# Kernel tuning notes

Measured on AMD Instinct MI355X. Metric: run time of the kernel, lower is better.

Reference implementation:

```python
import jax, jax.numpy as jnp
import numpy as np


def lga_once(x, w, r):
    """One pass of local guided aggregation (GANet LGA).

    x: [B, D, H, W] cost volume
    w: [B, 3*k*k, H, W] per-pixel guidance weights (k = 2r+1); the three
       k*k groups weight disparity planes d, d-1, d+1 respectively.
    out[b,d,h,w] = sum_{i,j in kxk window}
        w0[b,ij,h,w] * x[b, d,   h+i-r, w+j-r]
      + w1[b,ij,h,w] * x[b, d-1, h+i-r, w+j-r]
      + w2[b,ij,h,w] * x[b, d+1, h+i-r, w+j-r]
    with zero padding outside spatial and disparity bounds.
    """
    B, D, H, W = x.shape
    k = 2 * r + 1
    k2 = k * k
    w0 = w[:, 0 * k2:1 * k2]
    w1 = w[:, 1 * k2:2 * k2]
    w2 = w[:, 2 * k2:3 * k2]
    # disparity-shifted volumes: xm[:, d] = x[:, d-1], xp[:, d] = x[:, d+1]
    xm = jnp.pad(x, ((0, 0), (1, 0), (0, 0), (0, 0)))[:, :D]
    xp = jnp.pad(x, ((0, 0), (0, 1), (0, 0), (0, 0)))[:, 1:]
    spad = ((0, 0), (0, 0), (r, r), (r, r))
    x0p = jnp.pad(x, spad)
    xmp = jnp.pad(xm, spad)
    xpp = jnp.pad(xp, spad)
    out = jnp.zeros_like(x)
    idx = 0
    for i in range(k):          # small fixed kxk loop; data dims stay vectorized
        for j in range(k):
            p0 = x0p[:, :, i:i + H, j:j + W]
            pm = xmp[:, :, i:i + H, j:j + W]
            pp = xpp[:, :, i:i + H, j:j + W]
            out = out + (w0[:, idx:idx + 1] * p0
                         + w1[:, idx:idx + 1] * pm
                         + w2[:, idx:idx + 1] * pp)
            idx += 1
    return out


def setup_inputs() -> dict:
    key = jax.random.key(0)
    k1, k2 = jax.random.split(key)
    B, D, H, W = 2, 48, 320, 640
    r = 2
    kk = 2 * r + 1
    input1 = jax.random.normal(k1, (B, D, H, W), dtype=jnp.float32)
    input2 = jax.random.uniform(k2, (B, 3 * kk * kk, H, W), dtype=jnp.float32)
    return {"input1": input1, "input2": input2, "radius": r}


def reference(input1, input2, radius):
    # LGA2 = local guided aggregation applied twice with the same weights
    y = lga_once(input1, input2, radius)
    return lga_once(y, input2, radius)
```

## Files before the change

kernel.cpp:

```cpp
#include <hip/hip_runtime.h>

namespace {
constexpr int Bn = 2, Dn = 48, Hn = 320, Wn = 640;
constexpr int R = 2, K = 5, K2 = 25, C3 = 75;
constexpr int TW = 64, TH = 4;
constexpr int LW = TW + 2 * R;
constexpr int LH = TH + 2 * R;
constexpr int NT = TW * TH;
constexpr int LTOT = LH * LW;
constexpr int LTOTP = 576;
constexpr int NSLOT = 8;
}

#define BARRIER(N) \
    asm volatile("s_waitcnt vmcnt(" #N ") lgkmcnt(0)\n\ts_barrier" ::: "memory")

__global__ __launch_bounds__(NT, 2)
void lga_pass(const float* __restrict__ x, const float* __restrict__ wt,
              float* __restrict__ out) {
    __shared__ __align__(16) float pl[NSLOT][LTOTP];

    const int tx = threadIdx.x;
    const int ty = threadIdx.y;
    const int tid = ty * TW + tx;

    const int w0pix = blockIdx.x * TW;
    const int h0pix = blockIdx.y * TH;
    const int b = blockIdx.z;

    const int gw = w0pix + tx;
    const int gh = h0pix + ty;

    const size_t ps = (size_t)Hn * Wn;

    int soff[3];
#pragma unroll
    for (int t = 0; t < 3; ++t) {
        int idx = tid + t * NT;
        int rr = idx / LW;
        int cc = idx - rr * LW;
        int hh = h0pix - R + rr;
        int ww = w0pix - R + cc;
        bool ok = (idx < LTOT) && hh >= 0 && hh < Hn && ww >= 0 && ww < Wn;
        soff[t] = ok ? (hh * Wn + ww) : 0;
    }

    const float* xb = x + (size_t)b * Dn * ps;
    const int wseg = tid & ~63;

    float wr[C3];
    {
        const float* wp = wt + (size_t)b * C3 * ps + (size_t)gh * Wn + gw;
#pragma unroll
        for (int c = 0; c < C3; ++c) wr[c] = wp[(size_t)c * ps];
#pragma unroll
        for (int i = 0; i < K; ++i) {
            const int hh = gh + i - R;
            const bool vh = (hh >= 0) && (hh < Hn);
#pragma unroll
            for (int j = 0; j < K; ++j) {
                const int ww = gw + j - R;
                if (!(vh && ww >= 0 && ww < Wn)) {
                    wr[i * K + j] = 0.f;
                    wr[K2 + i * K + j] = 0.f;
                    wr[2 * K2 + i * K + j] = 0.f;
                }
            }
        }
    }

    float* op = out + (size_t)b * Dn * ps + (size_t)gh * Wn + gw;
    const int lbase = ty * LW + tx;

    auto dma = [&](int p, int slot) {
        if (p >= Dn) return;
        const float* src = xb + (size_t)p * ps;
        __builtin_amdgcn_global_load_lds(
            (const __attribute__((address_space(1))) void*)(src + soff[0]),
            (__attribute__((address_space(3))) void*)(&pl[slot][0 * NT + wseg]),
            4, 0, 0);
        __builtin_amdgcn_global_load_lds(
            (const __attribute__((address_space(1))) void*)(src + soff[1]),
            (__attribute__((address_space(3))) void*)(&pl[slot][1 * NT + wseg]),
            4, 0, 0);
        if (ty == 0) {
            __builtin_amdgcn_global_load_lds(
                (const __attribute__((address_space(1))) void*)(src + soff[2]),
                (__attribute__((address_space(3))) void*)(&pl[slot][2 * NT + tx]),
                4, 0, 0);
        }
    };

    float carry = 0.f, s1prev = 0.f;

    auto step = [&](int p, int sR, int sD) {
        dma(p + 6, sD);
        float S0 = 0.f, S1 = 0.f, S2 = 0.f;
#pragma unroll
        for (int i = 0; i < K; ++i) {
            float v0 = pl[sR][lbase + i * LW + 0];
            float v1 = pl[sR][lbase + i * LW + 1];
            float v2 = pl[sR][lbase + i * LW + 2];
            float v3 = pl[sR][lbase + i * LW + 3];
            float v4 = pl[sR][lbase + i * LW + 4];
            S0 += wr[i*K+0]*v0 + wr[i*K+1]*v1 + wr[i*K+2]*v2 + wr[i*K+3]*v3 + wr[i*K+4]*v4;
            S1 += wr[K2+i*K+0]*v0 + wr[K2+i*K+1]*v1 + wr[K2+i*K+2]*v2 + wr[K2+i*K+3]*v3 + wr[K2+i*K+4]*v4;
            S2 += wr[2*K2+i*K+0]*v0 + wr[2*K2+i*K+1]*v1 + wr[2*K2+i*K+2]*v2 + wr[2*K2+i*K+3]*v3 + wr[2*K2+i*K+4]*v4;
        }
        if (p > 0) { *op = carry + S2; op += ps; }
        carry = S0 + s1prev;
        s1prev = S1;
    };

#pragma unroll
    for (int q = 0; q < 6; ++q) dma(q, q);
    BARRIER(8);

    for (int d0 = 0; d0 < 40; d0 += 8) {
        step(d0 + 0, 0, 6); step(d0 + 1, 1, 7); BARRIER(8);
        step(d0 + 2, 2, 0); step(d0 + 3, 3, 1); BARRIER(8);
        step(d0 + 4, 4, 2); step(d0 + 5, 5, 3); BARRIER(8);
        step(d0 + 6, 6, 4); step(d0 + 7, 7, 5); BARRIER(8);
    }
    step(40, 0, 6); step(41, 1, 7); BARRIER(8);
    step(42, 2, 0); step(43, 3, 1); BARRIER(4);
    step(44, 4, 2); step(45, 5, 3); BARRIER(0);
    step(46, 6, 4); step(47, 7, 5);
    *op = carry;
}

extern "C" void kernel_launch(void* const* d_in, const int* in_sizes, int n_in,
                              void* d_out, int out_size, void* d_ws, size_t ws_size,
                              hipStream_t stream) {
    const float* x = (const float*)d_in[0];
    const float* w = (const float*)d_in[1];
    float* out = (float*)d_out;
    float* tmp = (float*)d_ws;

    dim3 block(TW, TH, 1);
    dim3 grid(Wn / TW, Hn / TH, Bn);

    lga_pass<<<grid, block, 0, stream>>>(x, w, tmp);
    lga_pass<<<grid, block, 0, stream>>>(tmp, w, out);
}
```

Measured before the change: 380.4 us.

## Interleave disparity plane pairs as float2 in LDS to halve reads per plane

The shared-memory tile now holds two consecutive disparity planes interleaved as float2 in each slot. Each global_load_lds lane pair fetches the same pixel from adjacent planes. Each compute step reads one float2 per tap and accumulates two planes at once, which halves LDS read instructions and barriers per plane. The pipeline is rebuilt with 6 double-plane slots, new vmcnt thresholds, and a changed output-ordering scheme where the first step's S2a is written to plane D-1. This relies on the wraparound indexing and waitcnt counts being exactly right.

```diff
diff --git a/kernel.cpp b/kernel.cpp
--- a/kernel.cpp
+++ b/kernel.cpp
@@ -5,11 +5,10 @@
 constexpr int R = 2, K = 5, K2 = 25, C3 = 75;
 constexpr int TW = 64, TH = 4;
 constexpr int LW = TW + 2 * R;
-constexpr int LH = TH + 2 * R;
 constexpr int NT = TW * TH;
-constexpr int LTOT = LH * LW;
-constexpr int LTOTP = 576;
-constexpr int NSLOT = 8;
+constexpr int LTOT = 544;
+constexpr int SPAD = 640;
+constexpr int NSLOT = 6;
 }
 
 #define BARRIER(N) \
@@ -18,11 +17,10 @@
 __global__ __launch_bounds__(NT, 2)
 void lga_pass(const float* __restrict__ x, const float* __restrict__ wt,
               float* __restrict__ out) {
-    __shared__ __align__(16) float pl[NSLOT][LTOTP];
+    __shared__ float2 pl2[NSLOT][SPAD];
 
     const int tx = threadIdx.x;
     const int ty = threadIdx.y;
-    const int tid = ty * TW + tx;
 
     const int w0pix = blockIdx.x * TW;
     const int h0pix = blockIdx.y * TH;
@@ -33,20 +31,20 @@
 
     const size_t ps = (size_t)Hn * Wn;
 
-    int soff[3];
+    int soffA[5];
 #pragma unroll
-    for (int t = 0; t < 3; ++t) {
-        int idx = tid + t * NT;
-        int rr = idx / LW;
-        int cc = idx - rr * LW;
+    for (int t = 0; t < 5; ++t) {
+        int s = ty * 160 + t * 32 + (tx >> 1);
+        int rr = s / LW;
+        int cc = s - rr * LW;
         int hh = h0pix - R + rr;
         int ww = w0pix - R + cc;
-        bool ok = (idx < LTOT) && hh >= 0 && hh < Hn && ww >= 0 && ww < Wn;
-        soff[t] = ok ? (hh * Wn + ww) : 0;
+        bool ok = (s < LTOT) && hh >= 0 && hh < Hn && ww >= 0 && ww < Wn;
+        soffA[t] = ok ? (hh * Wn + ww) : 0;
     }
 
     const float* xb = x + (size_t)b * Dn * ps;
-    const int wseg = tid & ~63;
+    const float* xq = xb + (size_t)(tx & 1) * ps;
 
     float wr[C3];
     {
@@ -72,60 +70,60 @@
     float* op = out + (size_t)b * Dn * ps + (size_t)gh * Wn + gw;
     const int lbase = ty * LW + tx;
 
-    auto dma = [&](int p, int slot) {
-        if (p >= Dn) return;
-        const float* src = xb + (size_t)p * ps;
-        __builtin_amdgcn_global_load_lds(
-            (const __attribute__((address_space(1))) void*)(src + soff[0]),
-            (__attribute__((address_space(3))) void*)(&pl[slot][0 * NT + wseg]),
-            4, 0, 0);
-        __builtin_amdgcn_global_load_lds(
-            (const __attribute__((address_space(1))) void*)(src + soff[1]),
-            (__attribute__((address_space(3))) void*)(&pl[slot][1 * NT + wseg]),
-            4, 0, 0);
-        if (ty == 0) {
+    auto dma = [&](const float* pbase, int slot) {
+#pragma unroll
+        for (int t = 0; t < 5; ++t) {
             __builtin_amdgcn_global_load_lds(
-                (const __attribute__((address_space(1))) void*)(src + soff[2]),
-                (__attribute__((address_space(3))) void*)(&pl[slot][2 * NT + tx]),
+                (const __attribute__((address_space(1))) void*)(pbase + soffA[t]),
+                (__attribute__((address_space(3))) void*)(&pl2[slot][ty * 160 + t * 32]),
                 4, 0, 0);
         }
     };
 
     float carry = 0.f, s1prev = 0.f;
+    const float* pref = xq;
 
-    auto step = [&](int p, int sR, int sD) {
-        dma(p + 6, sD);
-        float S0 = 0.f, S1 = 0.f, S2 = 0.f;
+    dma(pref, 0); pref += 2 * ps;
+    dma(pref, 1); pref += 2 * ps;
+    dma(pref, 2); pref += 2 * ps;
+
+    auto stepc = [&](int slot, bool issue, bool first) {
+        if (issue) { dma(pref, (slot + 3 >= NSLOT) ? slot - 3 : slot + 3); pref += 2 * ps; }
+        float S0a = 0.f, S1a = 0.f, S2a = 0.f;
+        float S0b = 0.f, S1b = 0.f, S2b = 0.f;
+        const float2* wb = &pl2[slot][lbase];
 #pragma unroll
-        for (int i = 0; i < K; ++i) {
-            float v0 = pl[sR][lbase + i * LW + 0];
-            float v1 = pl[sR][lbase + i * LW + 1];
-            float v2 = pl[sR][lbase + i * LW + 2];
-            float v3 = pl[sR][lbase + i * LW + 3];
-            float v4 = pl[sR][lbase + i * LW + 4];
-            S0 += wr[i*K+0]*v0 + wr[i*K+1]*v1 + wr[i*K+2]*v2 + wr[i*K+3]*v3 + wr[i*K+4]*v4;
-            S1 += wr[K2+i*K+0]*v0 + wr[K2+i*K+1]*v1 + wr[K2+i*K+2]*v2 + wr[K2+i*K+3]*v3 + wr[K2+i*K+4]*v4;
-            S2 += wr[2*K2+i*K+0]*v0 + wr[2*K2+i*K+1]*v1 + wr[2*K2+i*K+2]*v2 + wr[2*K2+i*K+3]*v3 + wr[2*K2+i*K+4]*v4;
-        }
-        if (p > 0) { *op = carry + S2; op += ps; }
-        carry = S0 + s1prev;
-        s1prev = S1;
+        for (int i = 0; i < K; ++i)
+#pragma unroll
+            for (int j = 0; j < K; ++j) {
+                float2 v = wb[i * LW + j];
+                float w0 = wr[i * K + j];
+                float w1 = wr[K2 + i * K + j];
+                float w2 = wr[2 * K2 + i * K + j];
+                S0a += w0 * v.x; S1a += w1 * v.x; S2a += w2 * v.x;
+                S0b += w0 * v.y; S1b += w1 * v.y; S2b += w2 * v.y;
+            }
+        if (first) op[(size_t)(Dn - 1) * ps] = carry + S2a;
+        else       { *op = carry + S2a; op += ps; }
+        carry = S0a + s1prev; s1prev = S1a;
+        *op = carry + S2b; op += ps;
+        carry = S0b + s1prev; s1prev = S1b;
     };
 
-#pragma unroll
-    for (int q = 0; q < 6; ++q) dma(q, q);
-    BARRIER(8);
-
-    for (int d0 = 0; d0 < 40; d0 += 8) {
-        step(d0 + 0, 0, 6); step(d0 + 1, 1, 7); BARRIER(8);
-        step(d0 + 2, 2, 0); step(d0 + 3, 3, 1); BARRIER(8);
-        step(d0 + 4, 4, 2); step(d0 + 5, 5, 3); BARRIER(8);
-        step(d0 + 6, 6, 4); step(d0 + 7, 7, 5); BARRIER(8);
+    BARRIER(10); stepc(0, true, true);
+    BARRIER(12); stepc(1, true, false);
+    BARRIER(14); stepc(2, true, false);
+    for (int g = 0; g < 3; ++g) {
+        BARRIER(16); stepc(3, true, false);
+        BARRIER(16); stepc(4, true, false);
+        BARRIER(16); stepc(5, true, false);
+        BARRIER(16); stepc(0, true, false);
+        BARRIER(16); stepc(1, true, false);
+        BARRIER(16); stepc(2, true, false);
     }
-    step(40, 0, 6); step(41, 1, 7); BARRIER(8);
-    step(42, 2, 0); step(43, 3, 1); BARRIER(4);
-    step(44, 4, 2); step(45, 5, 3); BARRIER(0);
-    step(46, 6, 4); step(47, 7, 5);
+    BARRIER(16); stepc(3, false, false);
+    BARRIER(11); stepc(4, false, false);
+    BARRIER(6);  stepc(5, false, false);
     *op = carry;
 }
 
```

After: 457.6 us. 20.3% more time.
